# Kernel optimization log

Measured on AMD Instinct MI355X. Metric: run time of the kernel, lower is better.

The kernel has to match this reference:

```python
import jax, jax.numpy as jnp
import numpy as np

NEG_INF = -1e30  # masked-softmax sentinel (exactly reproduces index_select+softmax)


def _pool(lbh, mask, scorer_w, layer_w):
    # lbh: [L, T, H]; mask: [T] bool selecting the pooled positions.
    # Masked softmax over positions == softmax over index_select'ed positions.
    scores = jnp.einsum('lth,ch->ltc', lbh, scorer_w)            # [L, T, C]
    scores = jnp.where(mask[None, :, None], scores, NEG_INF)
    attn = jax.nn.softmax(scores, axis=1)                        # zero at masked pos
    pooled = jnp.einsum('lth,ltc->lch', lbh, attn)               # [L, C, H]
    combined = jnp.einsum('l,lch->ch', layer_w, pooled)          # [C, H]
    return combined.reshape(-1)                                  # [C*H]


def reference(hidden_states, input_ids, layer_logits, scorer_w, hte_token_id, d_token_ids, window):
    layers = hidden_states[1:]                                   # [L, B, T, H]
    L, B, T, H = layers.shape
    ar = jnp.arange(T)
    layer_w = jax.nn.softmax(layer_logits)                       # [L]

    # HTE window mask: first occurrence of hte_token_id (else T-1), pos..pos+window
    is_hte = input_ids == hte_token_id                           # [B, T]
    pos = jnp.where(is_hte.any(-1), jnp.argmax(is_hte, axis=-1), T - 1)  # [B]
    win_mask = (ar[None, :] >= pos[:, None]) & (ar[None, :] <= pos[:, None] + window)

    # Descriptor mask: any position matching any d_token_id; fallback = position 0
    desc = (input_ids[:, :, None] == d_token_ids[None, None, :]).any(-1)  # [B, T]
    desc_mask = jnp.where(desc.any(-1, keepdims=True), desc, ar[None, :] == 0)

    layers_b = jnp.transpose(layers, (1, 0, 2, 3))               # [B, L, T, H]
    pool = jax.vmap(lambda lbh, m: _pool(lbh, m, scorer_w, layer_w))
    pooled_hte = pool(layers_b, win_mask)                        # [B, C*H]
    pooled_desc = pool(layers_b, desc_mask)                      # [B, C*H]
    return jnp.concatenate([pooled_hte, pooled_desc], axis=-1)   # [B, 2*C*H]


def setup_inputs() -> dict:
    key = jax.random.key(0)
    k_h, k_ids, k_ll, k_w = jax.random.split(key, 4)
    NUM_LAYERS, B, T, H, C, VOCAB = 12, 8, 2048, 768, 4, 512
    return {
        'hidden_states': jax.random.normal(k_h, (NUM_LAYERS + 1, B, T, H), dtype=jnp.float32),
        'input_ids': jax.random.randint(k_ids, (B, T), 0, VOCAB, dtype=jnp.int64),
        'layer_logits': jax.random.normal(k_ll, (NUM_LAYERS,), dtype=jnp.float32),
        'scorer_w': jax.random.normal(k_w, (C, H), dtype=jnp.float32) * 0.02,
        'hte_token_id': 5,
        'd_token_ids': jnp.arange(3, dtype=jnp.int64),
        'window': 4,
    }
```

## Files before the change

### kernel.cpp

```cpp
#include <hip/hip_runtime.h>

#define TPB 256
#define CMAX 8

__global__ void mha_agg_kernel(const float* __restrict__ hidden,
                               const int* __restrict__ ids,
                               const float* __restrict__ layer_logits,
                               const float* __restrict__ scorer_w,
                               const int* __restrict__ hte_id_p,
                               const int* __restrict__ d_tok,
                               const int* __restrict__ window_p,
                               float* __restrict__ out,
                               int L, int B, int T, int H, int C, int ND)
{
    const int bid  = blockIdx.x;
    const int l    = bid % L;
    const int m    = (bid / L) & 1;
    const int b    = bid / (2 * L);
    const int tid  = threadIdx.x;
    const int wave = tid >> 6;
    const int lane = tid & 63;

    extern __shared__ unsigned char smem_raw[];
    unsigned short* s_sel    = (unsigned short*)smem_raw;
    float*          s_scores = (float*)(smem_raw + ((2 * T + 15) & ~15));
    float*          s_sw     = s_scores + (size_t)T * C;
    int*            s_misc   = (int*)(s_sw + (size_t)C * H);

    if (tid == 0) { s_misc[0] = T; s_misc[1] = 0; }
    for (int i = tid; i < C * H; i += TPB) s_sw[i] = scorer_w[i];
    __syncthreads();

    const int* idrow = ids + (size_t)b * T;
    if (m == 0) {
        const int hte = hte_id_p[0];
        for (int t = tid; t < T; t += TPB)
            if (idrow[t] == hte) atomicMin(&s_misc[0], t);
        __syncthreads();
        if (tid == 0) {
            int pos = s_misc[0]; if (pos >= T) pos = T - 1;
            int win = window_p[0];
            int hi = pos + win; if (hi > T - 1) hi = T - 1;
            int n = hi - pos + 1;
            for (int i = 0; i < n; i++) s_sel[i] = (unsigned short)(pos + i);
            s_misc[1] = n;
        }
    } else {
        int dt[CMAX];
        for (int d = 0; d < ND; d++) dt[d] = d_tok[d];
        for (int t = tid; t < T; t += TPB) {
            int v = idrow[t];
            bool hit = false;
            for (int d = 0; d < ND; d++) hit = hit || (v == dt[d]);
            if (hit) { int idx = atomicAdd(&s_misc[1], 1); s_sel[idx] = (unsigned short)t; }
        }
        __syncthreads();
        if (tid == 0 && s_misc[1] == 0) { s_sel[0] = 0; s_misc[1] = 1; }
    }
    __syncthreads();
    const int n = s_misc[1];

    float mx = -3.402823466e38f;
    for (int j = 0; j < L; j++) mx = fmaxf(mx, layer_logits[j]);
    float den = 0.f;
    for (int j = 0; j < L; j++) den += expf(layer_logits[j] - mx);
    const float lwl = expf(layer_logits[l] - mx) / den;

    const float* base = hidden + ((size_t)(l + 1) * B + b) * (size_t)T * H;

    for (int i = wave; i < n; i += TPB / 64) {
        const float* row = base + (size_t)s_sel[i] * H;
        float p[CMAX];
        for (int c = 0; c < C; c++) p[c] = 0.f;
        for (int h = lane; h < H; h += 64) {
            float v = row[h];
            for (int c = 0; c < C; c++) p[c] += v * s_sw[c * H + h];
        }
        for (int off = 32; off; off >>= 1)
            for (int c = 0; c < C; c++) p[c] += __shfl_down(p[c], off);
        if (lane == 0)
            for (int c = 0; c < C; c++) s_scores[i * C + c] = p[c];
    }
    __syncthreads();

    for (int c = wave; c < C; c += TPB / 64) {
        float smax = -3.402823466e38f;
        for (int i = lane; i < n; i += 64) smax = fmaxf(smax, s_scores[i * C + c]);
        for (int off = 32; off; off >>= 1) smax = fmaxf(smax, __shfl_xor(smax, off));
        float ssum = 0.f;
        for (int i = lane; i < n; i += 64) {
            float e = expf(s_scores[i * C + c] - smax);
            s_scores[i * C + c] = e;
            ssum += e;
        }
        for (int off = 32; off; off >>= 1) ssum += __shfl_xor(ssum, off);
        const float scale = lwl / ssum;
        for (int i = lane; i < n; i += 64) s_scores[i * C + c] *= scale;
    }
    __syncthreads();

    float* obase = out + ((size_t)b * 2 + m) * (size_t)C * H;
    for (int h = tid; h < H; h += TPB) {
        float a[CMAX];
        for (int c = 0; c < C; c++) a[c] = 0.f;
        for (int i = 0; i < n; i++) {
            float v = base[(size_t)s_sel[i] * H + h];
            for (int c = 0; c < C; c++) a[c] += s_scores[i * C + c] * v;
        }
        for (int c = 0; c < C; c++) atomicAdd(obase + c * H + h, a[c]);
    }
}

extern "C" void kernel_launch(void* const* d_in, const int* in_sizes, int n_in,
                              void* d_out, int out_size, void* d_ws, size_t ws_size,
                              hipStream_t stream) {
    const float* hidden = (const float*)d_in[0];
    const int*   ids    = (const int*)d_in[1];
    const float* ll     = (const float*)d_in[2];
    const float* sw     = (const float*)d_in[3];
    const int*   hte    = (const int*)d_in[4];
    const int*   dtok   = (const int*)d_in[5];
    const int*   win    = (const int*)d_in[6];
    float*       out    = (float*)d_out;

    const int L  = in_sizes[2];
    const int CH = in_sizes[3];
    const int B  = out_size / (2 * CH);
    const int T  = in_sizes[1] / B;
    const int H  = (int)((long long)in_sizes[0] / ((long long)(L + 1) * in_sizes[1]));
    const int C  = CH / H;
    const int ND = in_sizes[5];

    hipMemsetAsync(d_out, 0, (size_t)out_size * sizeof(float), stream);

    const size_t smem = (size_t)((2 * T + 15) & ~15)
                      + (size_t)T * C * sizeof(float)
                      + (size_t)CH * sizeof(float)
                      + 16;
    mha_agg_kernel<<<B * 2 * L, TPB, smem, stream>>>(hidden, ids, ll, sw, hte, dtok, win, out,
                                                     L, B, T, H, C, ND);
}
```

Measured before the change: 765.0 us.

## Fuse layer loop into one block per batch and mask, drop atomics and memset

Each block now handles one (batch, mask) pair and loops over all layers, accumulating the weighted pooled output in registers with 1024 threads. Per-position mask construction and scorer weight loading happen once instead of per layer. Output is written directly, which removes the atomicAdds and the zeroing memset. In exchange the grid shrinks to 16 blocks and the layers are processed serially, which reduces parallelism and exposes more memory latency.

```diff
diff --git a/kernel.cpp b/kernel.cpp
--- a/kernel.cpp
+++ b/kernel.cpp
@@ -1,25 +1,28 @@
 #include <hip/hip_runtime.h>
 
-#define TPB 256
+#define TPB 1024
 #define CMAX 8
+#define LMAX 16
+#define HI_MAX 2
 
-__global__ void mha_agg_kernel(const float* __restrict__ hidden,
-                               const int* __restrict__ ids,
-                               const float* __restrict__ layer_logits,
-                               const float* __restrict__ scorer_w,
-                               const int* __restrict__ hte_id_p,
-                               const int* __restrict__ d_tok,
-                               const int* __restrict__ window_p,
-                               float* __restrict__ out,
-                               int L, int B, int T, int H, int C, int ND)
+__global__ __launch_bounds__(TPB) void mha_agg_fused(
+        const float* __restrict__ hidden,
+        const int* __restrict__ ids,
+        const float* __restrict__ layer_logits,
+        const float* __restrict__ scorer_w,
+        const int* __restrict__ hte_id_p,
+        const int* __restrict__ d_tok,
+        const int* __restrict__ window_p,
+        float* __restrict__ out,
+        int L, int B, int T, int H, int C, int ND)
 {
     const int bid  = blockIdx.x;
-    const int l    = bid % L;
-    const int m    = (bid / L) & 1;
-    const int b    = bid / (2 * L);
+    const int m    = bid & 1;
+    const int b    = bid >> 1;
     const int tid  = threadIdx.x;
     const int wave = tid >> 6;
     const int lane = tid & 63;
+    const int NW   = TPB / 64;
 
     extern __shared__ unsigned char smem_raw[];
     unsigned short* s_sel    = (unsigned short*)smem_raw;
@@ -41,9 +44,9 @@
             int pos = s_misc[0]; if (pos >= T) pos = T - 1;
             int win = window_p[0];
             int hi = pos + win; if (hi > T - 1) hi = T - 1;
-            int n = hi - pos + 1;
-            for (int i = 0; i < n; i++) s_sel[i] = (unsigned short)(pos + i);
-            s_misc[1] = n;
+            int nn = hi - pos + 1;
+            for (int i = 0; i < nn; i++) s_sel[i] = (unsigned short)(pos + i);
+            s_misc[1] = nn;
         }
     } else {
         int dt[CMAX];
@@ -60,55 +63,76 @@
     __syncthreads();
     const int n = s_misc[1];
 
+    float lw[LMAX];
     float mx = -3.402823466e38f;
-    for (int j = 0; j < L; j++) mx = fmaxf(mx, layer_logits[j]);
+    for (int j = 0; j < L; j++) { lw[j] = layer_logits[j]; mx = fmaxf(mx, lw[j]); }
     float den = 0.f;
-    for (int j = 0; j < L; j++) den += expf(layer_logits[j] - mx);
-    const float lwl = expf(layer_logits[l] - mx) / den;
+    for (int j = 0; j < L; j++) { lw[j] = expf(lw[j] - mx); den += lw[j]; }
+    const float iden = 1.f / den;
 
-    const float* base = hidden + ((size_t)(l + 1) * B + b) * (size_t)T * H;
+    float acc0[CMAX];
+    float acc1[CMAX];
+    for (int c = 0; c < C; c++) { acc0[c] = 0.f; acc1[c] = 0.f; }
 
-    for (int i = wave; i < n; i += TPB / 64) {
-        const float* row = base + (size_t)s_sel[i] * H;
-        float p[CMAX];
-        for (int c = 0; c < C; c++) p[c] = 0.f;
-        for (int h = lane; h < H; h += 64) {
-            float v = row[h];
-            for (int c = 0; c < C; c++) p[c] += v * s_sw[c * H + h];
+    for (int l = 0; l < L; l++) {
+        const float* base = hidden + ((size_t)(l + 1) * B + b) * (size_t)T * H;
+
+        for (int i = wave; i < n; i += NW) {
+            const float* row = base + (size_t)s_sel[i] * H;
+            float p[CMAX];
+            for (int c = 0; c < C; c++) p[c] = 0.f;
+            for (int h = lane; h < H; h += 64) {
+                float v = row[h];
+                for (int c = 0; c < C; c++) p[c] += v * s_sw[c * H + h];
+            }
+            for (int off = 32; off; off >>= 1)
+                for (int c = 0; c < C; c++) p[c] += __shfl_down(p[c], off);
+            if (lane == 0)
+                for (int c = 0; c < C; c++) s_scores[i * C + c] = p[c];
         }
-        for (int off = 32; off; off >>= 1)
-            for (int c = 0; c < C; c++) p[c] += __shfl_down(p[c], off);
-        if (lane == 0)
-            for (int c = 0; c < C; c++) s_scores[i * C + c] = p[c];
+        __syncthreads();
+
+        const float lwl = lw[l] * iden;
+        for (int c = wave; c < C; c += NW) {
+            float smax = -3.402823466e38f;
+            for (int i = lane; i < n; i += 64) smax = fmaxf(smax, s_scores[i * C + c]);
+            for (int off = 32; off; off >>= 1) smax = fmaxf(smax, __shfl_xor(smax, off));
+            float ssum = 0.f;
+            for (int i = lane; i < n; i += 64) {
+                float e = expf(s_scores[i * C + c] - smax);
+                s_scores[i * C + c] = e;
+                ssum += e;
+            }
+            for (int off = 32; off; off >>= 1) ssum += __shfl_xor(ssum, off);
+            const float scale = lwl / ssum;
+            for (int i = lane; i < n; i += 64) s_scores[i * C + c] *= scale;
+        }
+        __syncthreads();
+
+        {
+            const int h0 = tid;
+            if (h0 < H) {
+                for (int i = 0; i < n; i++) {
+                    float v = base[(size_t)s_sel[i] * H + h0];
+                    for (int c = 0; c < C; c++) acc0[c] += s_scores[i * C + c] * v;
+                }
+            }
+            const int h1 = tid + TPB;
+            if (h1 < H) {
+                for (int i = 0; i < n; i++) {
+                    float v = base[(size_t)s_sel[i] * H + h1];
+                    for (int c = 0; c < C; c++) acc1[c] += s_scores[i * C + c] * v;
+                }
+            }
+        }
+        __syncthreads();
     }
-    __syncthreads();
-
-    for (int c = wave; c < C; c += TPB / 64) {
-        float smax = -3.402823466e38f;
-        for (int i = lane; i < n; i += 64) smax = fmaxf(smax, s_scores[i * C + c]);
-        for (int off = 32; off; off >>= 1) smax = fmaxf(smax, __shfl_xor(smax, off));
-        float ssum = 0.f;
-        for (int i = lane; i < n; i += 64) {
-            float e = expf(s_scores[i * C + c] - smax);
-            s_scores[i * C + c] = e;
-            ssum += e;
-        }
-        for (int off = 32; off; off >>= 1) ssum += __shfl_xor(ssum, off);
-        const float scale = lwl / ssum;
-        for (int i = lane; i < n; i += 64) s_scores[i * C + c] *= scale;
-    }
-    __syncthreads();
 
     float* obase = out + ((size_t)b * 2 + m) * (size_t)C * H;
-    for (int h = tid; h < H; h += TPB) {
-        float a[CMAX];
-        for (int c = 0; c < C; c++) a[c] = 0.f;
-        for (int i = 0; i < n; i++) {
-            float v = base[(size_t)s_sel[i] * H + h];
-            for (int c = 0; c < C; c++) a[c] += s_scores[i * C + c] * v;
-        }
-        for (int c = 0; c < C; c++) atomicAdd(obase + c * H + h, a[c]);
-    }
+    if (tid < H)
+        for (int c = 0; c < C; c++) obase[c * H + tid] = acc0[c];
+    if (tid + TPB < H)
+        for (int c = 0; c < C; c++) obase[c * H + tid + TPB] = acc1[c];
 }
 
 extern "C" void kernel_launch(void* const* d_in, const int* in_sizes, int n_in,
@@ -131,12 +155,11 @@
     const int C  = CH / H;
     const int ND = in_sizes[5];
 
-    hipMemsetAsync(d_out, 0, (size_t)out_size * sizeof(float), stream);
-
     const size_t smem = (size_t)((2 * T + 15) & ~15)
                       + (size_t)T * C * sizeof(float)
                       + (size_t)CH * sizeof(float)
                       + 16;
-    mha_agg_kernel<<<B * 2 * L, TPB, smem, stream>>>(hidden, ids, ll, sw, hte, dtok, win, out,
-                                                     L, B, T, H, C, ND);
+
+    mha_agg_fused<<<B * 2, TPB, smem, stream>>>(hidden, ids, ll, sw, hte, dtok, win, out,
+                                                L, B, T, H, C, ND);
 }
```

New measurement: 1.032 ms. +34.9%, slower.

## Replace atomic output accumulation with per-layer partials plus reduce kernel, vectorize loads

Applied to the files above, without the earlier changes.

Each block now writes its per-layer pooled contribution to a workspace buffer, and a second kernel sums the partials over layers. This replaces the memset and the global float atomics. Row loads in the scoring and pooling loops now use float4 when alignment allows. The cost is an extra kernel launch and a workspace round trip of B*2*L*C*H floats, and the old atomic path is kept as a fallback when no workspace is provided.

```diff
diff --git a/kernel.cpp b/kernel.cpp
--- a/kernel.cpp
+++ b/kernel.cpp
@@ -3,15 +3,16 @@
 #define TPB 256
 #define CMAX 8
 
-__global__ void mha_agg_kernel(const float* __restrict__ hidden,
-                               const int* __restrict__ ids,
-                               const float* __restrict__ layer_logits,
-                               const float* __restrict__ scorer_w,
-                               const int* __restrict__ hte_id_p,
-                               const int* __restrict__ d_tok,
-                               const int* __restrict__ window_p,
-                               float* __restrict__ out,
-                               int L, int B, int T, int H, int C, int ND)
+__global__ void mha_part_kernel(const float* __restrict__ hidden,
+                                const int* __restrict__ ids,
+                                const float* __restrict__ layer_logits,
+                                const float* __restrict__ scorer_w,
+                                const int* __restrict__ hte_id_p,
+                                const int* __restrict__ d_tok,
+                                const int* __restrict__ window_p,
+                                float* __restrict__ dst,
+                                int L, int B, int T, int H, int C, int ND,
+                                int atomic_mode)
 {
     const int bid  = blockIdx.x;
     const int l    = bid % L;
@@ -41,9 +42,9 @@
             int pos = s_misc[0]; if (pos >= T) pos = T - 1;
             int win = window_p[0];
             int hi = pos + win; if (hi > T - 1) hi = T - 1;
-            int n = hi - pos + 1;
-            for (int i = 0; i < n; i++) s_sel[i] = (unsigned short)(pos + i);
-            s_misc[1] = n;
+            int nn = hi - pos + 1;
+            for (int i = 0; i < nn; i++) s_sel[i] = (unsigned short)(pos + i);
+            s_misc[1] = nn;
         }
     } else {
         int dt[CMAX];
@@ -67,14 +68,27 @@
     const float lwl = expf(layer_logits[l] - mx) / den;
 
     const float* base = hidden + ((size_t)(l + 1) * B + b) * (size_t)T * H;
+    const bool vec4 = ((H & 3) == 0) && (((T * C) & 3) == 0);
 
     for (int i = wave; i < n; i += TPB / 64) {
         const float* row = base + (size_t)s_sel[i] * H;
         float p[CMAX];
         for (int c = 0; c < C; c++) p[c] = 0.f;
-        for (int h = lane; h < H; h += 64) {
-            float v = row[h];
-            for (int c = 0; c < C; c++) p[c] += v * s_sw[c * H + h];
+        if (vec4) {
+            const float4* row4 = (const float4*)row;
+            const int H4 = H >> 2;
+            for (int h4 = lane; h4 < H4; h4 += 64) {
+                const float4 v = row4[h4];
+                for (int c = 0; c < C; c++) {
+                    const float4 w = *(const float4*)(s_sw + (size_t)c * H + (h4 << 2));
+                    p[c] += v.x * w.x + v.y * w.y + v.z * w.z + v.w * w.w;
+                }
+            }
+        } else {
+            for (int h = lane; h < H; h += 64) {
+                float v = row[h];
+                for (int c = 0; c < C; c++) p[c] += v * s_sw[c * H + h];
+            }
         }
         for (int off = 32; off; off >>= 1)
             for (int c = 0; c < C; c++) p[c] += __shfl_down(p[c], off);
@@ -99,16 +113,62 @@
     }
     __syncthreads();
 
-    float* obase = out + ((size_t)b * 2 + m) * (size_t)C * H;
-    for (int h = tid; h < H; h += TPB) {
-        float a[CMAX];
-        for (int c = 0; c < C; c++) a[c] = 0.f;
-        for (int i = 0; i < n; i++) {
-            float v = base[(size_t)s_sel[i] * H + h];
-            for (int c = 0; c < C; c++) a[c] += s_scores[i * C + c] * v;
-        }
-        for (int c = 0; c < C; c++) atomicAdd(obase + c * H + h, a[c]);
-    }
+    if (atomic_mode) {
+        float* obase = dst + ((size_t)b * 2 + m) * (size_t)C * H;
+        for (int h = tid; h < H; h += TPB) {
+            float a[CMAX];
+            for (int c = 0; c < C; c++) a[c] = 0.f;
+            for (int i = 0; i < n; i++) {
+                float v = base[(size_t)s_sel[i] * H + h];
+                for (int c = 0; c < C; c++) a[c] += s_scores[i * C + c] * v;
+            }
+            for (int c = 0; c < C; c++) atomicAdd(obase + c * H + h, a[c]);
+        }
+    } else {
+        float* pbase = dst + (size_t)bid * C * H;
+        if (vec4) {
+            const int H4 = H >> 2;
+            for (int h4 = tid; h4 < H4; h4 += TPB) {
+                float4 a[CMAX];
+                for (int c = 0; c < C; c++) a[c] = make_float4(0.f, 0.f, 0.f, 0.f);
+                for (int i = 0; i < n; i++) {
+                    const float4 v = *(const float4*)(base + (size_t)s_sel[i] * H + (h4 << 2));
+                    for (int c = 0; c < C; c++) {
+                        const float s = s_scores[i * C + c];
+                        a[c].x += s * v.x; a[c].y += s * v.y;
+                        a[c].z += s * v.z; a[c].w += s * v.w;
+                    }
+                }
+                for (int c = 0; c < C; c++)
+                    *(float4*)(pbase + (size_t)c * H + (h4 << 2)) = a[c];
+            }
+        } else {
+            for (int h = tid; h < H; h += TPB) {
+                float a[CMAX];
+                for (int c = 0; c < C; c++) a[c] = 0.f;
+                for (int i = 0; i < n; i++) {
+                    float v = base[(size_t)s_sel[i] * H + h];
+                    for (int c = 0; c < C; c++) a[c] += s_scores[i * C + c] * v;
+                }
+                for (int c = 0; c < C; c++) pbase[c * H + h] = a[c];
+            }
+        }
+    }
+}
+
+__global__ void mha_reduce_kernel(const float* __restrict__ part,
+                                  float* __restrict__ out,
+                                  int L, int CH, int total)
+{
+    const int i = blockIdx.x * blockDim.x + threadIdx.x;
+    if (i >= total) return;
+    const int bm = i / CH;
+    const int ch = i - bm * CH;
+    const float* p = part + (size_t)bm * L * CH + ch;
+    float s = 0.f;
+#pragma unroll 4
+    for (int l = 0; l < L; l++) s += p[(size_t)l * CH];
+    out[i] = s;
 }
 
 extern "C" void kernel_launch(void* const* d_in, const int* in_sizes, int n_in,
@@ -131,12 +191,24 @@
     const int C  = CH / H;
     const int ND = in_sizes[5];
 
-    hipMemsetAsync(d_out, 0, (size_t)out_size * sizeof(float), stream);
-
     const size_t smem = (size_t)((2 * T + 15) & ~15)
                       + (size_t)T * C * sizeof(float)
                       + (size_t)CH * sizeof(float)
                       + 16;
-    mha_agg_kernel<<<B * 2 * L, TPB, smem, stream>>>(hidden, ids, ll, sw, hte, dtok, win, out,
-                                                     L, B, T, H, C, ND);
+
+    const size_t part_bytes = (size_t)B * 2 * L * CH * sizeof(float);
+
+    if (d_ws != nullptr && ws_size >= part_bytes) {
+        mha_part_kernel<<<B * 2 * L, TPB, smem, stream>>>(
+            hidden, ids, ll, sw, hte, dtok, win, (float*)d_ws,
+            L, B, T, H, C, ND, 0);
+        const int total = B * 2 * CH;
+        mha_reduce_kernel<<<(total + 255) / 256, 256, 0, stream>>>(
+            (float*)d_ws, out, L, CH, total);
+    } else {
+        hipMemsetAsync(d_out, 0, (size_t)out_size * sizeof(float), stream);
+        mha_part_kernel<<<B * 2 * L, TPB, smem, stream>>>(
+            hidden, ids, ll, sw, hte, dtok, win, out,
+            L, B, T, H, C, ND, 1);
+    }
 }
```

Measured after the change: 738.0 us. 3.5% less time.
